# Kernel tuning notes

Measured on AMD Instinct MI355X. Metric: run time of the kernel, lower is better.

The kernel has to match this reference:

```python
import jax, jax.numpy as jnp
import numpy as np

N_NODES = 100000
D_FEAT = 128
N_EDGES = 500000
HIDDEN = 256
OUT = 1


def setup_inputs() -> dict:
    key = jax.random.key(0)
    k1, k2, k3, k4, k5, k6 = jax.random.split(key, 6)
    z = jax.random.normal(k1, (N_NODES, D_FEAT), dtype=jnp.float32)
    edge_index = jax.random.randint(k2, (N_EDGES, 3), 0, N_NODES, dtype=jnp.int64)
    # torch nn.Linear weights: [out, in]
    fc1_w = jax.random.normal(k3, (HIDDEN, 2 * D_FEAT), dtype=jnp.float32) * (1.0 / np.sqrt(2 * D_FEAT))
    fc1_b = jax.random.normal(k4, (HIDDEN,), dtype=jnp.float32) * 0.01
    fc2_w = jax.random.normal(k5, (OUT, HIDDEN), dtype=jnp.float32) * (1.0 / np.sqrt(HIDDEN))
    fc2_b = jax.random.normal(k6, (OUT,), dtype=jnp.float32) * 0.01
    return {"z": z, "edge_index": edge_index, "fc1_w": fc1_w, "fc1_b": fc1_b,
            "fc2_w": fc2_w, "fc2_b": fc2_b}


def reference(z, edge_index, fc1_w, fc1_b, fc2_w, fc2_b):
    row = edge_index[:, 1]
    col = edge_index[:, 2]
    concatenated = jnp.concatenate([z[row], z[col]], axis=1)  # [E, 2d]
    x = jax.nn.relu(concatenated @ fc1_w.T + fc1_b)           # [E, hidden]
    decoded = jax.nn.sigmoid(x @ fc2_w.T + fc2_b)             # [E, out]
    return decoded
```

## Files before the change

kernel.cpp:

```cpp
#include <hip/hip_runtime.h>
#include <stdint.h>

#define N_NODES 100000
#define D_FEAT  128
#define N_EDGES 500000
#define HIDDEN  256
#define EPT     64
#define NTILES  ((N_EDGES + EPT - 1) / EPT)
#define GRID_MAIN 256

typedef __bf16 bf16x8 __attribute__((ext_vector_type(8)));
typedef float  f32x4  __attribute__((ext_vector_type(4)));

__device__ __forceinline__ unsigned short f2bf(float f) {
  unsigned u = __builtin_bit_cast(unsigned, f);
  u += 0x7FFFu + ((u >> 16) & 1u);
  return (unsigned short)(u >> 16);
}

__device__ __forceinline__ uint4 pack8(float4 a, float4 b) {
  union { unsigned short s[8]; uint4 u; } o;
  o.s[0] = f2bf(a.x); o.s[1] = f2bf(a.y); o.s[2] = f2bf(a.z); o.s[3] = f2bf(a.w);
  o.s[4] = f2bf(b.x); o.s[5] = f2bf(b.y); o.s[6] = f2bf(b.z); o.s[7] = f2bf(b.w);
  return o.u;
}

__global__ __launch_bounds__(512, 2)
void mlp_fused(const int* __restrict__ eidx,
               const float* __restrict__ zf,
               const float* __restrict__ w1f,
               const float* __restrict__ b1,
               const float* __restrict__ w2g,
               const float* __restrict__ b2,
               float* __restrict__ out) {
  __shared__ unsigned char sbuf[3][EPT * 512];
  __shared__ float red[2][8][72];

  const int tid = threadIdx.x;
  const int w   = tid >> 6;
  const int l   = tid & 63;
  const int l15 = l & 15;
  const int g   = l >> 4;
  const int si  = w * 4;
  const int half = (l & 31) >> 4;

  const int is64 = (eidx[1] == 0 && eidx[3] == 0 && eidx[5] == 0);
  const float b2v = b2[0];

  bf16x8 a[2][8];
  #pragma unroll
  for (int rt = 0; rt < 2; ++rt) {
    const int n = w * 32 + rt * 16 + l15;
    #pragma unroll
    for (int ks = 0; ks < 8; ++ks) {
      const int k = ks * 32 + g * 8;
      const float4 lo = *(const float4*)(w1f + n * 256 + k);
      const float4 hi = *(const float4*)(w1f + n * 256 + k + 4);
      a[rt][ks] = __builtin_bit_cast(bf16x8, pack8(lo, hi));
    }
  }
  f32x4 b1v[2], w2v[2];
  #pragma unroll
  for (int rt = 0; rt < 2; ++rt) {
    const int nb = w * 32 + rt * 16 + g * 4;
    b1v[rt] = *(const f32x4*)(b1 + nb);
    w2v[rt] = *(const f32x4*)(w2g + nb);
  }

  auto gather = [&](int tt, float4* ga, float4* gb) {
    #pragma unroll
    for (int ii = 0; ii < 4; ++ii) {
      const int i = si + ii;
      const int m = 2 * i + (l >> 5);
      int e = tt * EPT + m;
      if (e >= N_EDGES) e = N_EDGES - 1;
      const int iv = is64 ? eidx[6 * e + 2 + 2 * half]
                          : eidx[3 * e + 1 + half];
      const int fof = ((l15 * 16) ^ ((m & 7) << 4)) >> 1;
      const float* src = zf + (size_t)iv * D_FEAT + fof;
      ga[ii] = *(const float4*)src;
      gb[ii] = *(const float4*)(src + 4);
    }
  };
  auto lds_write = [&](int buf, const float4* ga, const float4* gb) {
    #pragma unroll
    for (int ii = 0; ii < 4; ++ii) {
      const int i = si + ii;
      *(uint4*)&sbuf[buf][i * 1024 + l * 16] = pack8(ga[ii], gb[ii]);
    }
  };

  const int t0 = blockIdx.x;
  float4 ga[4], gb[4];
  gather(t0, ga, gb);
  lds_write(0, ga, gb);
  gather(t0 + GRID_MAIN, ga, gb);
  __syncthreads();

  int it = 0;
  for (int t = t0; t < NTILES; t += GRID_MAIN, ++it) {
    const int cb  = it % 3;
    const int par = it & 1;

    lds_write((it + 1) % 3, ga, gb);
    gather(t + 2 * GRID_MAIN, ga, gb);

    f32x4 acc[2][4];
    #pragma unroll
    for (int rt = 0; rt < 2; ++rt)
      #pragma unroll
      for (int ct = 0; ct < 4; ++ct)
        acc[rt][ct] = (f32x4){0.f, 0.f, 0.f, 0.f};

    const unsigned char* sb = &sbuf[cb][0];
    #pragma unroll
    for (int ks = 0; ks < 8; ++ks) {
      bf16x8 bf[4];
      #pragma unroll
      for (int ct = 0; ct < 4; ++ct) {
        const int m    = ct * 16 + l15;
        const int phys = m * 512 + ((ks * 64 + g * 16) ^ ((m & 7) << 4));
        bf[ct] = *(const bf16x8*)(sb + phys);
      }
      __builtin_amdgcn_s_setprio(1);
      #pragma unroll
      for (int rt = 0; rt < 2; ++rt)
        #pragma unroll
        for (int ct = 0; ct < 4; ++ct)
          acc[rt][ct] = __builtin_amdgcn_mfma_f32_16x16x32_bf16(
              a[rt][ks], bf[ct], acc[rt][ct], 0, 0, 0);
      __builtin_amdgcn_s_setprio(0);
    }

    float p[4] = {0.f, 0.f, 0.f, 0.f};
    #pragma unroll
    for (int rt = 0; rt < 2; ++rt) {
      #pragma unroll
      for (int r = 0; r < 4; ++r) {
        const float bb = b1v[rt][r], w2r = w2v[rt][r];
        #pragma unroll
        for (int ct = 0; ct < 4; ++ct) {
          float x = acc[rt][ct][r] + bb;
          x = fmaxf(x, 0.f);
          p[ct] = fmaf(x, w2r, p[ct]);
        }
      }
    }
    #pragma unroll
    for (int ct = 0; ct < 4; ++ct) {
      p[ct] += __shfl_xor(p[ct], 16);
      p[ct] += __shfl_xor(p[ct], 32);
    }
    if (l < 16) {
      #pragma unroll
      for (int ct = 0; ct < 4; ++ct) red[par][w][ct * 16 + l] = p[ct];
    }

    __syncthreads();

    {
      const int el = 8 * w + (l & 7);
      float v = red[par][l >> 3][el];
      v += __shfl_xor(v, 8);
      v += __shfl_xor(v, 16);
      v += __shfl_xor(v, 32);
      const int e = t * EPT + el;
      if (l < 8 && e < N_EDGES)
        out[e] = 1.f / (1.f + __expf(-(v + b2v)));
    }
  }
}

extern "C" void kernel_launch(void* const* d_in, const int* in_sizes, int n_in,
                              void* d_out, int out_size, void* d_ws, size_t ws_size,
                              hipStream_t stream) {
  const float* z    = (const float*)d_in[0];
  const int*   eidx = (const int*)d_in[1];
  const float* fc1w = (const float*)d_in[2];
  const float* fc1b = (const float*)d_in[3];
  const float* fc2w = (const float*)d_in[4];
  const float* fc2b = (const float*)d_in[5];
  float* out = (float*)d_out;

  mlp_fused<<<GRID_MAIN, 512, 0, stream>>>(eidx, z, fc1w, fc1b, fc2w, fc2b, out);
}
```

Baseline: 176.2 us.

## Pre-convert node features to bf16 and gather via direct global-to-LDS loads

Adds a pre-pass kernel that converts z to bf16 in workspace, halving the bytes each gathered row costs. The main kernel then stages gathered rows straight into LDS with global_load_lds, skipping register staging and per-element conversion. It also reshapes the wave tiling to 4 N-tiles by 2 M-tiles per wave and defers the output reduction by one iteration, leaving a single barrier per tile. In exchange it adds an extra full pass over z (about 51 MB read, 25 MB written) every call, and the LDS layout loses its XOR swizzle, which may cause bank conflicts.

```diff
diff --git a/kernel.cpp b/kernel.cpp
--- a/kernel.cpp
+++ b/kernel.cpp
@@ -10,163 +10,178 @@
 #define GRID_MAIN 256
 
 typedef __bf16 bf16x8 __attribute__((ext_vector_type(8)));
+typedef __bf16 bf16x4 __attribute__((ext_vector_type(4)));
 typedef float  f32x4  __attribute__((ext_vector_type(4)));
 
-__device__ __forceinline__ unsigned short f2bf(float f) {
-  unsigned u = __builtin_bit_cast(unsigned, f);
-  u += 0x7FFFu + ((u >> 16) & 1u);
-  return (unsigned short)(u >> 16);
-}
-
-__device__ __forceinline__ uint4 pack8(float4 a, float4 b) {
-  union { unsigned short s[8]; uint4 u; } o;
-  o.s[0] = f2bf(a.x); o.s[1] = f2bf(a.y); o.s[2] = f2bf(a.z); o.s[3] = f2bf(a.w);
-  o.s[4] = f2bf(b.x); o.s[5] = f2bf(b.y); o.s[6] = f2bf(b.z); o.s[7] = f2bf(b.w);
-  return o.u;
+__device__ __forceinline__ void gld_lds16(const unsigned short* g, unsigned char* l) {
+  __builtin_amdgcn_global_load_lds(
+      (const __attribute__((address_space(1))) unsigned int*)g,
+      (__attribute__((address_space(3))) unsigned int*)l, 16, 0, 0);
+}
+
+__device__ __forceinline__ bf16x8 cvt8(f32x4 lo, f32x4 hi) {
+  bf16x8 r;
+  r[0] = (__bf16)lo[0]; r[1] = (__bf16)lo[1]; r[2] = (__bf16)lo[2]; r[3] = (__bf16)lo[3];
+  r[4] = (__bf16)hi[0]; r[5] = (__bf16)hi[1]; r[6] = (__bf16)hi[2]; r[7] = (__bf16)hi[3];
+  return r;
+}
+
+__global__ void cvt_z(const float* __restrict__ src, unsigned short* __restrict__ dst, int n4) {
+  int i = blockIdx.x * blockDim.x + threadIdx.x;
+  const int stride = gridDim.x * blockDim.x;
+  for (; i < n4; i += stride) {
+    const f32x4 v = ((const f32x4*)src)[i];
+    bf16x4 o;
+    o[0] = (__bf16)v[0]; o[1] = (__bf16)v[1]; o[2] = (__bf16)v[2]; o[3] = (__bf16)v[3];
+    ((bf16x4*)dst)[i] = o;
+  }
 }
 
 __global__ __launch_bounds__(512, 2)
-void mlp_fused(const int* __restrict__ eidx,
-               const float* __restrict__ zf,
-               const float* __restrict__ w1f,
-               const float* __restrict__ b1,
-               const float* __restrict__ w2g,
-               const float* __restrict__ b2,
-               float* __restrict__ out) {
+void mlp_main(const int* __restrict__ eidx,
+              const unsigned short* __restrict__ z16,
+              const float* __restrict__ w1f,
+              const float* __restrict__ b1,
+              const float* __restrict__ w2g,
+              const float* __restrict__ b2,
+              float* __restrict__ out) {
   __shared__ unsigned char sbuf[3][EPT * 512];
-  __shared__ float red[2][8][72];
-
-  const int tid = threadIdx.x;
-  const int w   = tid >> 6;
-  const int l   = tid & 63;
-  const int l15 = l & 15;
-  const int g   = l >> 4;
-  const int si  = w * 4;
-  const int half = (l & 31) >> 4;
+  __shared__ float red[2][4][72];
+
+  const int tid  = threadIdx.x;
+  const int w    = tid >> 6;
+  const int l    = tid & 63;
+  const int l15  = l & 15;
+  const int g    = l >> 4;
+  const int ng   = w >> 1;
+  const int mg   = w & 1;
+  const int half = w >> 2;
 
   const int is64 = (eidx[1] == 0 && eidx[3] == 0 && eidx[5] == 0);
   const float b2v = b2[0];
 
-  bf16x8 a[2][8];
+  bf16x8 a[4][8];
   #pragma unroll
-  for (int rt = 0; rt < 2; ++rt) {
-    const int n = w * 32 + rt * 16 + l15;
+  for (int nt = 0; nt < 4; ++nt) {
+    const int n = ng * 64 + nt * 16 + l15;
     #pragma unroll
     for (int ks = 0; ks < 8; ++ks) {
       const int k = ks * 32 + g * 8;
-      const float4 lo = *(const float4*)(w1f + n * 256 + k);
-      const float4 hi = *(const float4*)(w1f + n * 256 + k + 4);
-      a[rt][ks] = __builtin_bit_cast(bf16x8, pack8(lo, hi));
-    }
-  }
-  f32x4 b1v[2], w2v[2];
+      const f32x4 lo = *(const f32x4*)(w1f + n * 256 + k);
+      const f32x4 hi = *(const f32x4*)(w1f + n * 256 + k + 4);
+      a[nt][ks] = cvt8(lo, hi);
+    }
+  }
+  f32x4 b1v[4], w2v[4];
   #pragma unroll
-  for (int rt = 0; rt < 2; ++rt) {
-    const int nb = w * 32 + rt * 16 + g * 4;
-    b1v[rt] = *(const f32x4*)(b1 + nb);
-    w2v[rt] = *(const f32x4*)(w2g + nb);
-  }
-
-  auto gather = [&](int tt, float4* ga, float4* gb) {
-    #pragma unroll
-    for (int ii = 0; ii < 4; ++ii) {
-      const int i = si + ii;
-      const int m = 2 * i + (l >> 5);
-      int e = tt * EPT + m;
-      if (e >= N_EDGES) e = N_EDGES - 1;
-      const int iv = is64 ? eidx[6 * e + 2 + 2 * half]
-                          : eidx[3 * e + 1 + half];
-      const int fof = ((l15 * 16) ^ ((m & 7) << 4)) >> 1;
-      const float* src = zf + (size_t)iv * D_FEAT + fof;
-      ga[ii] = *(const float4*)src;
-      gb[ii] = *(const float4*)(src + 4);
-    }
+  for (int nt = 0; nt < 4; ++nt) {
+    const int nb = ng * 64 + nt * 16 + g * 4;
+    b1v[nt] = *(const f32x4*)(b1 + nb);
+    w2v[nt] = *(const f32x4*)(w2g + nb);
+  }
+
+  auto ldidx = [&](int t) -> int {
+    int e = t * EPT + l;
+    if (e > N_EDGES - 1) e = N_EDGES - 1;
+    return is64 ? eidx[6 * e + 2 + 2 * half] : eidx[3 * e + 1 + half];
   };
-  auto lds_write = [&](int buf, const float4* ga, const float4* gb) {
-    #pragma unroll
-    for (int ii = 0; ii < 4; ++ii) {
-      const int i = si + ii;
-      *(uint4*)&sbuf[buf][i * 1024 + l * 16] = pack8(ga[ii], gb[ii]);
+  auto stage = [&](int buf, int iv) {
+    const unsigned short* src = z16 + (size_t)iv * D_FEAT;
+    #pragma unroll
+    for (int j = 0; j < 4; ++j) {
+      const int c = 4 * w + j;
+      gld_lds16(src + ((c & 15) << 3), &sbuf[buf][c << 10]);
     }
   };
 
   const int t0 = blockIdx.x;
-  float4 ga[4], gb[4];
-  gather(t0, ga, gb);
-  lds_write(0, ga, gb);
-  gather(t0 + GRID_MAIN, ga, gb);
-  __syncthreads();
-
-  int it = 0;
+  int ivq = ldidx(t0);
+  stage(0, ivq);
+  int iv_next = ldidx(t0 + GRID_MAIN);
+
+  int cb = 0, it = 0;
   for (int t = t0; t < NTILES; t += GRID_MAIN, ++it) {
-    const int cb  = it % 3;
-    const int par = it & 1;
-
-    lds_write((it + 1) % 3, ga, gb);
-    gather(t + 2 * GRID_MAIN, ga, gb);
-
-    f32x4 acc[2][4];
-    #pragma unroll
-    for (int rt = 0; rt < 2; ++rt)
+    __syncthreads();
+
+    int cn = cb + 1; if (cn == 3) cn = 0;
+    stage(cn, iv_next);
+    iv_next = ldidx(t + 2 * GRID_MAIN);
+
+    if (it) {
+      if (w < 4) {
+        const int e = (w << 4) + (l >> 2);
+        float v = red[(it - 1) & 1][l & 3][e];
+        v += __shfl_xor(v, 1);
+        v += __shfl_xor(v, 2);
+        const int eg = (t - GRID_MAIN) * EPT + e;
+        if ((l & 3) == 0 && eg < N_EDGES)
+          out[eg] = 1.f / (1.f + __expf(-(v + b2v)));
+      }
+    }
+
+    f32x4 acc[4][2];
+    #pragma unroll
+    for (int nt = 0; nt < 4; ++nt) {
+      acc[nt][0] = (f32x4){0.f, 0.f, 0.f, 0.f};
+      acc[nt][1] = (f32x4){0.f, 0.f, 0.f, 0.f};
+    }
+    const unsigned char* sb = &sbuf[cb][0];
+    #pragma unroll
+    for (int ks = 0; ks < 8; ++ks) {
+      bf16x8 bf[2];
       #pragma unroll
-      for (int ct = 0; ct < 4; ++ct)
-        acc[rt][ct] = (f32x4){0.f, 0.f, 0.f, 0.f};
-
-    const unsigned char* sb = &sbuf[cb][0];
-    #pragma unroll
-    for (int ks = 0; ks < 8; ++ks) {
-      bf16x8 bf[4];
-      #pragma unroll
-      for (int ct = 0; ct < 4; ++ct) {
-        const int m    = ct * 16 + l15;
-        const int phys = m * 512 + ((ks * 64 + g * 16) ^ ((m & 7) << 4));
-        bf[ct] = *(const bf16x8*)(sb + phys);
+      for (int ct = 0; ct < 2; ++ct) {
+        const int c = ks * 4 + g;
+        const int m = mg * 32 + ct * 16 + l15;
+        bf[ct] = *(const bf16x8*)(sb + (c << 10) + (m << 4));
       }
       __builtin_amdgcn_s_setprio(1);
       #pragma unroll
-      for (int rt = 0; rt < 2; ++rt)
+      for (int nt = 0; nt < 4; ++nt)
         #pragma unroll
-        for (int ct = 0; ct < 4; ++ct)
-          acc[rt][ct] = __builtin_amdgcn_mfma_f32_16x16x32_bf16(
-              a[rt][ks], bf[ct], acc[rt][ct], 0, 0, 0);
+        for (int ct = 0; ct < 2; ++ct)
+          acc[nt][ct] = __builtin_amdgcn_mfma_f32_16x16x32_bf16(
+              a[nt][ks], bf[ct], acc[nt][ct], 0, 0, 0);
       __builtin_amdgcn_s_setprio(0);
     }
 
-    float p[4] = {0.f, 0.f, 0.f, 0.f};
-    #pragma unroll
-    for (int rt = 0; rt < 2; ++rt) {
+    float p[2] = {0.f, 0.f};
+    #pragma unroll
+    for (int nt = 0; nt < 4; ++nt) {
       #pragma unroll
       for (int r = 0; r < 4; ++r) {
-        const float bb = b1v[rt][r], w2r = w2v[rt][r];
+        const float bb = b1v[nt][r], ww = w2v[nt][r];
         #pragma unroll
-        for (int ct = 0; ct < 4; ++ct) {
-          float x = acc[rt][ct][r] + bb;
+        for (int ct = 0; ct < 2; ++ct) {
+          float x = acc[nt][ct][r] + bb;
           x = fmaxf(x, 0.f);
-          p[ct] = fmaf(x, w2r, p[ct]);
+          p[ct] = fmaf(x, ww, p[ct]);
         }
       }
     }
     #pragma unroll
-    for (int ct = 0; ct < 4; ++ct) {
+    for (int ct = 0; ct < 2; ++ct) {
       p[ct] += __shfl_xor(p[ct], 16);
       p[ct] += __shfl_xor(p[ct], 32);
     }
     if (l < 16) {
-      #pragma unroll
-      for (int ct = 0; ct < 4; ++ct) red[par][w][ct * 16 + l] = p[ct];
-    }
-
-    __syncthreads();
-
-    {
-      const int el = 8 * w + (l & 7);
-      float v = red[par][l >> 3][el];
-      v += __shfl_xor(v, 8);
-      v += __shfl_xor(v, 16);
-      v += __shfl_xor(v, 32);
-      const int e = t * EPT + el;
-      if (l < 8 && e < N_EDGES)
-        out[e] = 1.f / (1.f + __expf(-(v + b2v)));
+      red[it & 1][ng][mg * 32 + l]      = p[0];
+      red[it & 1][ng][mg * 32 + 16 + l] = p[1];
+    }
+    cb = cn;
+  }
+
+  __syncthreads();
+  {
+    const int tl = t0 + (it - 1) * GRID_MAIN;
+    if (w < 4) {
+      const int e = (w << 4) + (l >> 2);
+      float v = red[(it - 1) & 1][l & 3][e];
+      v += __shfl_xor(v, 1);
+      v += __shfl_xor(v, 2);
+      const int eg = tl * EPT + e;
+      if ((l & 3) == 0 && eg < N_EDGES)
+        out[eg] = 1.f / (1.f + __expf(-(v + b2v)));
     }
   }
 }
@@ -182,5 +197,8 @@
   const float* fc2b = (const float*)d_in[5];
   float* out = (float*)d_out;
 
-  mlp_fused<<<GRID_MAIN, 512, 0, stream>>>(eidx, z, fc1w, fc1b, fc2w, fc2b, out);
-}
+  unsigned short* z16 = (unsigned short*)d_ws;
+
+  cvt_z<<<2048, 256, 0, stream>>>(z, z16, N_NODES * D_FEAT / 4);
+  mlp_main<<<GRID_MAIN, 512, 0, stream>>>(eidx, z16, fc1w, fc1b, fc2w, fc2b, out);
+}
```

New measurement: 215.3 us. 22.2% more time.
